# Kernel optimization log

Measured on AMD Instinct MI355X. Metric: run time of the kernel, lower is better.

Reference implementation:

```python
import jax, jax.numpy as jnp
import numpy as np

B, S, D_MODEL, N_HEADS = 4, 2048, 1024, 16
HEAD_DIM = D_MODEL // N_HEADS


def setup_inputs() -> dict:
    key = jax.random.key(0)
    k_x, k_wqkv, k_bqkv, k_wout, k_bout = jax.random.split(key, 5)
    x = jax.random.normal(k_x, (B, S, D_MODEL), dtype=jnp.float32)
    # causal mask: True = masked (matches masked_fill semantics)
    mask = jnp.triu(jnp.ones((S, S), dtype=bool), k=1)[None, None, :, :]
    sc = 1.0 / np.sqrt(D_MODEL)
    w_qkv = jax.random.normal(k_wqkv, (3 * D_MODEL, D_MODEL), dtype=jnp.float32) * sc
    b_qkv = jax.random.normal(k_bqkv, (3 * D_MODEL,), dtype=jnp.float32) * 0.02
    w_out = jax.random.normal(k_wout, (D_MODEL, D_MODEL), dtype=jnp.float32) * sc
    b_out = jax.random.normal(k_bout, (D_MODEL,), dtype=jnp.float32) * 0.02
    return {"x": x, "mask": mask, "w_qkv": w_qkv, "b_qkv": b_qkv,
            "w_out": w_out, "b_out": b_out}


def reference(x, mask, w_qkv, b_qkv, w_out, b_out):
    b, s, d = x.shape
    qkv = x @ w_qkv.T + b_qkv                      # [B,S,3*D]
    qkv = qkv.reshape(b, s, 3, N_HEADS, HEAD_DIM)
    q = qkv[:, :, 0].transpose(0, 2, 1, 3)         # [B,H,S,Dh]
    k = qkv[:, :, 1].transpose(0, 2, 1, 3)
    v = qkv[:, :, 2].transpose(0, 2, 1, 3)
    scores = jnp.einsum('bhqd,bhkd->bhqk', q, k) / np.sqrt(HEAD_DIM)
    scores = jnp.where(mask, -jnp.inf, scores)
    attn = jax.nn.softmax(scores, axis=-1)         # dropout p=0.0 -> identity
    ctx = jnp.einsum('bhqk,bhkd->bhqd', attn, v)   # [B,H,S,Dh]
    ctx = ctx.transpose(0, 2, 1, 3).reshape(b, s, d)
    return ctx @ w_out.T + b_out
```

## Files before the change

### kernel.cpp

```cpp
#include <hip/hip_runtime.h>
#include <stdint.h>

typedef __attribute__((ext_vector_type(8))) short bf16x8;
typedef __attribute__((ext_vector_type(4))) float f32x4;
typedef unsigned short u16;

#define NUM_B 4
#define SEQ   2048
#define DM    1024
#define NH    16
#define DH    64
#define M_TOT (NUM_B * SEQ)

__device__ __forceinline__ float bf2f(u16 u) {
    union { unsigned int i; float f; } c; c.i = ((unsigned int)u) << 16; return c.f;
}
__device__ __forceinline__ u16 f2bf(float f) {
    union { float f; unsigned int i; } c; c.f = f;
    unsigned int u = c.i;
    return (u16)((u + 0x7FFFu + ((u >> 16) & 1u)) >> 16);
}
__device__ __forceinline__ unsigned int pack2(float a, float b) {
    return (unsigned int)f2bf(a) | ((unsigned int)f2bf(b) << 16);
}

#define GLOAD_LDS16(g, l)                                                     \
    __builtin_amdgcn_global_load_lds(                                         \
        (const __attribute__((address_space(1))) void*)(g),                   \
        (__attribute__((address_space(3))) void*)(l), 16, 0, 0)

__global__ void detect_dtype(const u16* __restrict__ x, int* __restrict__ flag) {
    __shared__ int cnt;
    if (threadIdx.x == 0) cnt = 0;
    __syncthreads();
    int local = 0;
    for (int i = threadIdx.x; i < 4096; i += 256) {
        const u16 v = x[i];
        const int e = (v >> 7) & 0xFF;
        if (v == 0 || (e >= 110 && e <= 145)) local++;
    }
    atomicAdd(&cnt, local);
    __syncthreads();
    if (threadIdx.x == 0) *flag = (cnt >= 3686) ? 0 : 1;
}

__global__ void convert_bf16(const void* __restrict__ in, u16* __restrict__ out,
                             long n, const int* __restrict__ flag)
{
    const long i0 = ((long)blockIdx.x * 256 + threadIdx.x) * 8;
    const long stride = (long)gridDim.x * 256 * 8;
    if (*flag) {
        const float* f = (const float*)in;
        for (long i = i0; i < n; i += stride) {
            float4 a = *(const float4*)(f + i);
            float4 b = *(const float4*)(f + i + 4);
            uint4 o;
            o.x = pack2(a.x, a.y); o.y = pack2(a.z, a.w);
            o.z = pack2(b.x, b.y); o.w = pack2(b.z, b.w);
            *(uint4*)(out + i) = o;
        }
    } else {
        const uint4* s = (const uint4*)in;
        for (long i = i0; i < n; i += stride)
            *(uint4*)(out + i) = s[i >> 3];
    }
}

template <int MODE, int N_TOT>
__global__ __launch_bounds__(256) void gemm_bt(
    const u16* __restrict__ A, const u16* __restrict__ Bm,
    const u16* __restrict__ bias,
    void* __restrict__ out0v, u16* __restrict__ out1, u16* __restrict__ out2,
    const int* __restrict__ outf32, long out_off)
{
    __shared__ __align__(16) u16 As[128 * 32];
    __shared__ __align__(16) u16 Bs[128 * 32];
    const int K = 1024;

    const int tid  = threadIdx.x;
    const int wave = tid >> 6;
    const int lane = tid & 63;
    const int l15  = lane & 15;
    const int quad = lane >> 4;

    const int m0 = blockIdx.y * 128;
    const int n0 = blockIdx.x * 128;
    const int wm = (wave >> 1) * 64;
    const int wn = (wave & 1) * 64;

    const int srow = lane >> 2;
    const int soff = (lane & 3) * 8;

    f32x4 acc[4][4];
#pragma unroll
    for (int i = 0; i < 4; ++i)
#pragma unroll
        for (int j = 0; j < 4; ++j)
            acc[i][j] = (f32x4){0.f, 0.f, 0.f, 0.f};

    for (int k0 = 0; k0 < K; k0 += 32) {
#pragma unroll
        for (int r = 0; r < 2; ++r) {
            const int chunk = wave * 2 + r;
            const int row   = chunk * 16 + srow;
            GLOAD_LDS16(&A[(size_t)(m0 + row) * K + k0 + soff], &As[chunk * 512]);
            GLOAD_LDS16(&Bm[(size_t)(n0 + row) * K + k0 + soff], &Bs[chunk * 512]);
        }
        __syncthreads();

        bf16x8 af[4], bfv[4];
#pragma unroll
        for (int i = 0; i < 4; ++i)
            af[i] = *(const bf16x8*)(&As[(wm + i * 16 + l15) * 32 + quad * 8]);
#pragma unroll
        for (int j = 0; j < 4; ++j)
            bfv[j] = *(const bf16x8*)(&Bs[(wn + j * 16 + l15) * 32 + quad * 8]);

#pragma unroll
        for (int i = 0; i < 4; ++i)
#pragma unroll
            for (int j = 0; j < 4; ++j)
                acc[i][j] = __builtin_amdgcn_mfma_f32_16x16x32_bf16(
                    af[i], bfv[j], acc[i][j], 0, 0, 0);
        __syncthreads();
    }

    const int of32 = outf32 ? *outf32 : 0;
#pragma unroll
    for (int j = 0; j < 4; ++j) {
        const int n  = n0 + wn + j * 16 + l15;
        const float bv = bf2f(bias[n]);
#pragma unroll
        for (int i = 0; i < 4; ++i) {
#pragma unroll
            for (int reg = 0; reg < 4; ++reg) {
                const int m = m0 + wm + i * 16 + quad * 4 + reg;
                const float v = acc[i][j][reg] + bv;
                if (MODE == 0) {
                    const int sel = n >> 10;
                    const int h   = (n >> 6) & 15;
                    const int dh  = n & 63;
                    const int b   = m >> 11;
                    const int s   = m & 2047;
                    if (sel == 2) {
                        out2[((size_t)((b * NH + h) * DH + dh)) * SEQ + s] = f2bf(v);
                    } else {
                        u16* dst = (sel == 0) ? (u16*)out0v : out1;
                        dst[((size_t)((b * NH + h) * SEQ + s)) * DH + dh] = f2bf(v);
                    }
                } else {
                    if (of32)
                        ((float*)out0v)[out_off + (size_t)m * N_TOT + n] = v;
                    else
                        ((u16*)out0v)[out_off + (size_t)m * N_TOT + n] = f2bf(v);
                }
            }
        }
    }
}

__global__ __launch_bounds__(256) void attn_fwd(
    const u16* __restrict__ Qb, const u16* __restrict__ Kb,
    const u16* __restrict__ Vt, u16* __restrict__ ctx)
{
    __shared__ __align__(16) u16 Ks[2][2048];
    __shared__ __align__(16) u16 Vs[2][2048];
    __shared__ __align__(16) short Pbuf[4][2][16 * 40];

    const int tid  = threadIdx.x;
    const int wave = tid >> 6;
    const int lane = tid & 63;
    const int l15  = lane & 15;
    const int quad = lane >> 4;

    const int bh = blockIdx.x;
    const int q0 = blockIdx.y * 128;
    const int qrowA = q0 + wave * 32;
    const size_t base  = (size_t)bh * SEQ * DH;
    const size_t baseT = (size_t)bh * DH * SEQ;
    const float scale = 0.125f;

    bf16x8 qf[2][2];
#pragma unroll
    for (int f = 0; f < 2; ++f)
#pragma unroll
        for (int c = 0; c < 2; ++c)
            qf[f][c] = *(const bf16x8*)(&Qb[base + (size_t)(qrowA + f * 16 + l15) * DH + c * 32 + quad * 8]);

    f32x4 acc[2][4];
#pragma unroll
    for (int f = 0; f < 2; ++f)
#pragma unroll
        for (int j = 0; j < 4; ++j) acc[f][j] = (f32x4){0.f, 0.f, 0.f, 0.f};
    float lsum[2][4] = {{0.f, 0.f, 0.f, 0.f}, {0.f, 0.f, 0.f, 0.f}};

    const int ktend = blockIdx.y * 4 + 3;
    const int mkt   = blockIdx.y * 4 + wave;

    const int k_r = (wave & 1) * 16 + l15;
    const int k_c = ((wave >> 1) * 4 + quad) * 8;
    const int v_dh = wave * 16 + l15;
    const int v_k  = quad * 8;

    {
        GLOAD_LDS16(&Kb[base + (size_t)k_r * DH + k_c], &Ks[0][wave * 512]);
        GLOAD_LDS16(&Vt[baseT + (size_t)v_dh * SEQ + v_k], &Vs[0][wave * 512]);
    }

    for (int kt = 0; kt <= ktend; ++kt) {
        const int cur = kt & 1;
        __syncthreads();

        if (kt + 1 <= ktend) {
            const int nk0 = (kt + 1) * 32;
            GLOAD_LDS16(&Kb[base + (size_t)(nk0 + k_r) * DH + k_c],
                        &Ks[1 - cur][wave * 512]);
            GLOAD_LDS16(&Vt[baseT + (size_t)v_dh * SEQ + nk0 + v_k],
                        &Vs[1 - cur][wave * 512]);
        }

        if (kt <= mkt) {
            bf16x8 kf[2][2], vfr[4];
#pragma unroll
            for (int half = 0; half < 2; ++half)
#pragma unroll
                for (int c = 0; c < 2; ++c)
                    kf[half][c] = *(const bf16x8*)(&Ks[cur][(c * 2 + half) * 512 + lane * 8]);
#pragma unroll
            for (int j = 0; j < 4; ++j)
                vfr[j] = *(const bf16x8*)(&Vs[cur][j * 512 + lane * 8]);

            const int diag = (kt == mkt);
#pragma unroll
            for (int f = 0; f < 2; ++f) {
                f32x4 sc0 = (f32x4){0.f, 0.f, 0.f, 0.f};
                f32x4 sc1 = (f32x4){0.f, 0.f, 0.f, 0.f};
                sc0 = __builtin_amdgcn_mfma_f32_16x16x32_bf16(qf[f][0], kf[0][0], sc0, 0, 0, 0);
                sc0 = __builtin_amdgcn_mfma_f32_16x16x32_bf16(qf[f][1], kf[0][1], sc0, 0, 0, 0);
                sc1 = __builtin_amdgcn_mfma_f32_16x16x32_bf16(qf[f][0], kf[1][0], sc1, 0, 0, 0);
                sc1 = __builtin_amdgcn_mfma_f32_16x16x32_bf16(qf[f][1], kf[1][1], sc1, 0, 0, 0);

                float pa[4], pb[4];
                if (diag) {
#pragma unroll
                    for (int r = 0; r < 4; ++r) {
                        const int rr = quad * 4 + r;
                        if (f == 0) {
                            pa[r] = (l15 <= rr) ? __expf(sc0[r] * scale) : 0.f;
                            pb[r] = 0.f;
                        } else {
                            pa[r] = __expf(sc0[r] * scale);
                            pb[r] = (l15 <= rr) ? __expf(sc1[r] * scale) : 0.f;
                        }
                    }
                } else {
#pragma unroll
                    for (int r = 0; r < 4; ++r) {
                        pa[r] = __expf(sc0[r] * scale);
                        pb[r] = __expf(sc1[r] * scale);
                    }
                }
#pragma unroll
                for (int r = 0; r < 4; ++r)
                    lsum[f][r] += pa[r] + pb[r];

                short* pw = Pbuf[wave][f];
                asm volatile("" ::: "memory");
#pragma unroll
                for (int r = 0; r < 4; ++r) {
                    const int row = quad * 4 + r;
                    pw[row * 40 + l15]      = (short)f2bf(pa[r]);
                    pw[row * 40 + 16 + l15] = (short)f2bf(pb[r]);
                }
                asm volatile("" ::: "memory");
                const bf16x8 pf = *(const bf16x8*)(&pw[l15 * 40 + quad * 8]);

#pragma unroll
                for (int j = 0; j < 4; ++j)
                    acc[f][j] = __builtin_amdgcn_mfma_f32_16x16x32_bf16(pf, vfr[j], acc[f][j], 0, 0, 0);
            }
        }
    }

#pragma unroll
    for (int off = 1; off <= 8; off <<= 1)
#pragma unroll
        for (int f = 0; f < 2; ++f)
#pragma unroll
            for (int r = 0; r < 4; ++r)
                lsum[f][r] += __shfl_xor(lsum[f][r], off);

    const int b = bh >> 4;
    const int h = bh & 15;
#pragma unroll
    for (int f = 0; f < 2; ++f) {
#pragma unroll
        for (int r = 0; r < 4; ++r) {
            const float invL = 1.0f / lsum[f][r];
            const int qrow = qrowA + f * 16 + quad * 4 + r;
            const size_t rowaddr = ((size_t)(b * SEQ + qrow)) * DM + h * DH;
#pragma unroll
            for (int j = 0; j < 4; ++j)
                ctx[rowaddr + j * 16 + l15] = f2bf(acc[f][j][r] * invL);
        }
    }
}

extern "C" void kernel_launch(void* const* d_in, const int* in_sizes, int n_in,
                              void* d_out, int out_size, void* d_ws, size_t ws_size,
                              hipStream_t stream)
{
    auto find = [&](long want, int fb) -> const void* {
        for (int i = 0; i < n_in; ++i)
            if ((long)in_sizes[i] == want) return d_in[i];
        if (fb >= n_in) fb = n_in - 1;
        return d_in[fb];
    };
    const void* x     = find(8388608, 0);
    const void* w_qkv = find(3145728, 2);
    const void* b_qkv = find(3072,    3);
    const void* w_out = find(1048576, 4);
    const void* b_out = find(1024,    5);

    char* ws   = (char*)d_ws;
    int*  flag = (int*)ws;
    char* p    = ws + 256;

    u16* xbf    = (u16*)p;                 p += (size_t)8388608 * 2;
    u16* wqkvbf = (u16*)p;                 p += (size_t)3145728 * 2;
    u16* bqkvbf = (u16*)p;                 p += 8192;
    u16* woutbf = (u16*)p;                 p += (size_t)1048576 * 2;
    u16* boutbf = (u16*)p;                 p += 8192;

    const size_t tensor_bytes = (size_t)M_TOT * DM * sizeof(u16);
    const size_t chunk_bytes  = tensor_bytes / NUM_B;
    const size_t conv_end     = (size_t)(p - ws);

    detect_dtype<<<1, 256, 0, stream>>>((const u16*)x, flag);
    auto cgrid = [](long n) { long g = (n / 8 + 255) / 256; return (int)(g > 2048 ? 2048 : g); };
    convert_bf16<<<cgrid(8388608), 256, 0, stream>>>(x,     xbf,    8388608, flag);
    convert_bf16<<<cgrid(3145728), 256, 0, stream>>>(w_qkv, wqkvbf, 3145728, flag);
    convert_bf16<<<cgrid(3072),    256, 0, stream>>>(b_qkv, bqkvbf, 3072,    flag);
    convert_bf16<<<cgrid(1048576), 256, 0, stream>>>(w_out, woutbf, 1048576, flag);
    convert_bf16<<<cgrid(1024),    256, 0, stream>>>(b_out, boutbf, 1024,    flag);

    if (ws_size >= conv_end + 4 * tensor_bytes) {
        u16* Qb  = (u16*)(ws + conv_end);
        u16* Kb  = (u16*)(ws + conv_end + tensor_bytes);
        u16* Vb  = (u16*)(ws + conv_end + 2 * tensor_bytes);
        u16* ctx = (u16*)(ws + conv_end + 3 * tensor_bytes);

        gemm_bt<0, 3072><<<dim3(24, 64), 256, 0, stream>>>(
            xbf, wqkvbf, bqkvbf, Qb, Kb, Vb, nullptr, 0);
        attn_fwd<<<dim3(NUM_B * NH, SEQ / 128), 256, 0, stream>>>(Qb, Kb, Vb, ctx);
        gemm_bt<1, 1024><<<dim3(8, 64), 256, 0, stream>>>(
            ctx, woutbf, boutbf, d_out, nullptr, nullptr, flag, 0);
    } else {
        u16* Qb  = (u16*)(ws + conv_end);
        u16* Kb  = (u16*)(ws + conv_end + chunk_bytes);
        u16* Vb  = (u16*)(ws + conv_end + 2 * chunk_bytes);
        u16* ctx = (u16*)(ws + conv_end + 3 * chunk_bytes);
        for (int b = 0; b < NUM_B; ++b) {
            const long eoff = (long)b * SEQ * DM;
            gemm_bt<0, 3072><<<dim3(24, 16), 256, 0, stream>>>(
                xbf + eoff, wqkvbf, bqkvbf, Qb, Kb, Vb, nullptr, 0);
            attn_fwd<<<dim3(NH, SEQ / 128), 256, 0, stream>>>(Qb, Kb, Vb, ctx);
            gemm_bt<1, 1024><<<dim3(8, 16), 256, 0, stream>>>(
                ctx, woutbf, boutbf, d_out, nullptr, nullptr, flag, eoff);
        }
    }
}
```

Measured before the change: 345.2 us.

## Balance causal attention blocks by pairing query tiles and use exp2 with hardware bf16 convert

Each attention block now takes one 64-row query slab from the front of the sequence and one from the back, so every block has about the same number of causal key tiles. Before, blocks covering late queries did far more work than blocks covering early ones. The softmax exponent is folded into an exp2 with a prescaled log2e constant. The software round-to-nearest bf16 conversion is replaced with the v_cvt_pk_bf16_f32 instruction. Within a block, the waves on the low slab sit idle through the extra key tiles needed by the high slab, and the hardware conversion may round slightly differently.

```diff
diff --git a/kernel.cpp b/kernel.cpp
--- a/kernel.cpp
+++ b/kernel.cpp
@@ -23,6 +23,18 @@
 __device__ __forceinline__ unsigned int pack2(float a, float b) {
     return (unsigned int)f2bf(a) | ((unsigned int)f2bf(b) << 16);
 }
+
+__device__ __forceinline__ u16 f2bf_hw(float a) {
+    unsigned int r;
+    asm("v_cvt_pk_bf16_f32 %0, %1, %2" : "=v"(r) : "v"(a), "v"(0.0f));
+    return (u16)r;
+}
+
+#if __has_builtin(__builtin_amdgcn_exp2f)
+#define EXP2F __builtin_amdgcn_exp2f
+#else
+#define EXP2F exp2f
+#endif
 
 #define GLOAD_LDS16(g, l)                                                     \
     __builtin_amdgcn_global_load_lds(                                         \
@@ -174,11 +186,15 @@
     const int quad = lane >> 4;
 
     const int bh = blockIdx.x;
-    const int q0 = blockIdx.y * 128;
-    const int qrowA = q0 + wave * 32;
+    const int yb = blockIdx.y;
+    const int qrowA = (wave < 2) ? (yb * 64 + wave * 32)
+                                 : (1984 - yb * 64 + (wave - 2) * 32);
+    const int mkt   = qrowA >> 5;
+    const int ktend = 63 - 2 * yb;
+
     const size_t base  = (size_t)bh * SEQ * DH;
     const size_t baseT = (size_t)bh * DH * SEQ;
-    const float scale = 0.125f;
+    const float sc_l2e = 0.18033688011112042f;
 
     bf16x8 qf[2][2];
 #pragma unroll
@@ -193,9 +209,6 @@
 #pragma unroll
         for (int j = 0; j < 4; ++j) acc[f][j] = (f32x4){0.f, 0.f, 0.f, 0.f};
     float lsum[2][4] = {{0.f, 0.f, 0.f, 0.f}, {0.f, 0.f, 0.f, 0.f}};
-
-    const int ktend = blockIdx.y * 4 + 3;
-    const int mkt   = blockIdx.y * 4 + wave;
 
     const int k_r = (wave & 1) * 16 + l15;
     const int k_c = ((wave >> 1) * 4 + quad) * 8;
@@ -246,18 +259,18 @@
                     for (int r = 0; r < 4; ++r) {
                         const int rr = quad * 4 + r;
                         if (f == 0) {
-                            pa[r] = (l15 <= rr) ? __expf(sc0[r] * scale) : 0.f;
+                            pa[r] = (l15 <= rr) ? EXP2F(sc0[r] * sc_l2e) : 0.f;
                             pb[r] = 0.f;
                         } else {
-                            pa[r] = __expf(sc0[r] * scale);
-                            pb[r] = (l15 <= rr) ? __expf(sc1[r] * scale) : 0.f;
+                            pa[r] = EXP2F(sc0[r] * sc_l2e);
+                            pb[r] = (l15 <= rr) ? EXP2F(sc1[r] * sc_l2e) : 0.f;
                         }
                     }
                 } else {
 #pragma unroll
                     for (int r = 0; r < 4; ++r) {
-                        pa[r] = __expf(sc0[r] * scale);
-                        pb[r] = __expf(sc1[r] * scale);
+                        pa[r] = EXP2F(sc0[r] * sc_l2e);
+                        pb[r] = EXP2F(sc1[r] * sc_l2e);
                     }
                 }
 #pragma unroll
@@ -269,8 +282,8 @@
 #pragma unroll
                 for (int r = 0; r < 4; ++r) {
                     const int row = quad * 4 + r;
-                    pw[row * 40 + l15]      = (short)f2bf(pa[r]);
-                    pw[row * 40 + 16 + l15] = (short)f2bf(pb[r]);
+                    pw[row * 40 + l15]      = (short)f2bf_hw(pa[r]);
+                    pw[row * 40 + 16 + l15] = (short)f2bf_hw(pb[r]);
                 }
                 asm volatile("" ::: "memory");
                 const bf16x8 pf = *(const bf16x8*)(&pw[l15 * 40 + quad * 8]);
@@ -301,7 +314,7 @@
             const size_t rowaddr = ((size_t)(b * SEQ + qrow)) * DM + h * DH;
 #pragma unroll
             for (int j = 0; j < 4; ++j)
-                ctx[rowaddr + j * 16 + l15] = f2bf(acc[f][j][r] * invL);
+                ctx[rowaddr + j * 16 + l15] = f2bf_hw(acc[f][j][r] * invL);
         }
     }
 }
```

New measurement: 351.5 us. About the same (+1.8%).
